# Kernel tuning notes

Hardware: AMD Instinct MI355X
Metric: run time of the kernel (lower is better)

Reference implementation:

```python
import jax, jax.numpy as jnp
import numpy as np

B, N, C_IN = 4, 120000, 4
FEAT, H, W = 128, 128, 128
PC_RANGE = (-50.0, -50.0, -5.0, 50.0, 50.0, 3.0)
EPS = 1e-5  # BatchNorm eps (torch default)


def setup_inputs() -> dict:
    key = jax.random.key(0)
    ks = jax.random.split(key, 16)
    # LiDAR-like point cloud: x,y spread ~[-90,90] (mostly in-range), z ~[-6,6], intensity ~N(0,1)
    points = jax.random.normal(ks[0], (B, N, C_IN), jnp.float32) * jnp.array([30.0, 30.0, 2.0, 1.0], jnp.float32)

    def lin(k, o, i):
        return jax.random.normal(k, (o, i), jnp.float32) * (1.0 / np.sqrt(i))

    def bn(k, c):
        k1, k2, k3, k4 = jax.random.split(k, 4)
        return (jax.random.normal(k1, (c,), jnp.float32) * 0.1 + 1.0,  # gamma
                jax.random.normal(k2, (c,), jnp.float32) * 0.1,        # beta
                jax.random.normal(k3, (c,), jnp.float32) * 0.1,        # running mean
                jax.random.uniform(k4, (c,), jnp.float32, 0.5, 1.5))   # running var

    g1, be1, m1, v1 = bn(ks[3], 64)
    g2, be2, m2, v2 = bn(ks[4], 128)
    g3, be3, m3, v3 = bn(ks[5], FEAT)
    return {
        'points': points,
        'W1': lin(ks[6], 64, C_IN), 'b1': jax.random.normal(ks[7], (64,), jnp.float32) * 0.01,
        'g1': g1, 'be1': be1, 'm1': m1, 'v1': v1,
        'W2': lin(ks[8], 128, 64), 'b2': jax.random.normal(ks[9], (128,), jnp.float32) * 0.01,
        'g2': g2, 'be2': be2, 'm2': m2, 'v2': v2,
        'W3': lin(ks[10], FEAT, 128), 'b3': jax.random.normal(ks[11], (FEAT,), jnp.float32) * 0.01,
        'g3': g3, 'be3': be3, 'm3': m3, 'v3': v3,
    }


def _bn_relu(x, g, b, m, v):
    # eval-mode BatchNorm1d + ReLU, applied over last (channel) axis
    return jax.nn.relu((x - m) * jax.lax.rsqrt(v + EPS) * g + b)


def _forward(points, W1, b1, g1, be1, m1, v1, W2, b2, g2, be2, m2, v2, W3, b3, g3, be3, m3, v3):
    # Per-point MLP (1x1 convs == per-point linears): [B,N,4] -> [B,N,FEAT]
    h = _bn_relu(jnp.einsum('bni,oi->bno', points, W1) + b1, g1, be1, m1, v1)
    h = _bn_relu(jnp.einsum('bni,oi->bno', h, W2) + b2, g2, be2, m2, v2)
    feats = _bn_relu(jnp.einsum('bni,oi->bno', h, W3) + b3, g3, be3, m3, v3)  # [B,N,FEAT]

    x, y = points[..., 0], points[..., 1]
    x_norm = (x - PC_RANGE[0]) / (PC_RANGE[3] - PC_RANGE[0])
    y_norm = (y - PC_RANGE[1]) / (PC_RANGE[4] - PC_RANGE[1])
    valid = (x_norm >= 0) & (x_norm <= 1) & (y_norm >= 0) & (y_norm <= 1)  # [B,N]

    gx = jnp.clip((x_norm * (W - 1)).astype(jnp.int32), 0, W - 1)
    gy = jnp.clip((y_norm * (H - 1)).astype(jnp.int32), 0, H - 1)
    bidx = jnp.arange(B, dtype=jnp.int32)[:, None]
    # invalid points routed to a dummy segment B*H*W
    seg = jnp.where(valid, bidx * (H * W) + gy * W + gx, B * H * W)  # [B,N]

    bev = jax.ops.segment_max(feats.reshape(B * N, FEAT), seg.reshape(B * N),
                              num_segments=B * H * W + 1)  # [B*H*W+1, FEAT]
    bev = bev[:B * H * W]
    bev = jnp.where(jnp.isneginf(bev), jnp.zeros((), bev.dtype), bev)  # empty cells stay 0
    return bev.reshape(B, H, W, FEAT).transpose(0, 3, 1, 2)  # [B, FEAT, H, W]


def reference(points, W1, b1, g1, be1, m1, v1, W2, b2, g2, be2, m2, v2, W3, b3, g3, be3, m3, v3):
    return _forward(points, W1, b1, g1, be1, m1, v1, W2, b2, g2, be2, m2, v2, W3, b3, g3, be3, m3, v3)
```

## Files before the change

kernel.cpp:

```cpp
#include <hip/hip_runtime.h>
#include <hip/hip_fp16.h>

#define BB 4
#define NN 120000
#define FEAT 128
#define HH 128
#define WW 128
#define NPTS (BB*NN)
#define HW (HH*WW)

#define OW1    0
#define OB1    256
#define OW2P   320
#define OB2    4416
#define OW3P   4544
#define OB3    12736
#define OW3F   12864
#define OW2F   21056
#define OCNT   25152
#define OOFF   90688
#define ONV    156224
#define OCELLS 156288
#define OSIDX  636288
#define OSCELL 1116288
#define OFEATS 1596288
#define OBEV   1596288
#define BEV_ELEMS (BB*HW*FEAT)

#if defined(__has_builtin)
#if __has_builtin(__builtin_amdgcn_fdot2)
#define HAS_FDOT2 1
#endif
#endif

typedef _Float16 hv2 __attribute__((ext_vector_type(2)));
typedef _Float16 f16x8 __attribute__((ext_vector_type(8)));
typedef float    f32x4 __attribute__((ext_vector_type(4)));
typedef float    fv16  __attribute__((ext_vector_type(16)));

__device__ __forceinline__ unsigned pk2(float a, float b) {
    __half2 h = __floats2half2_rn(a, b);
    return __builtin_bit_cast(unsigned, h);
}

__device__ __forceinline__ float dot2(unsigned a, unsigned b, float c) {
#ifdef HAS_FDOT2
    return __builtin_amdgcn_fdot2(__builtin_bit_cast(hv2, a),
                                  __builtin_bit_cast(hv2, b), c, false);
#else
    __half2 ah = __builtin_bit_cast(__half2, a), bh = __builtin_bit_cast(__half2, b);
    c = fmaf(__low2float(ah), __low2float(bh), c);
    return fmaf(__high2float(ah), __high2float(bh), c);
#endif
}

__device__ __forceinline__ unsigned hmax2u(unsigned a, unsigned b) {
    unsigned al = a & 0xFFFFu, bl = b & 0xFFFFu;
    unsigned ah = a & 0xFFFF0000u, bh = b & 0xFFFF0000u;
    unsigned lo = (al > bl) ? al : bl;
    unsigned hi = (ah > bh) ? ah : bh;
    return lo | hi;
}

__global__ void fold_weights_k(
    const float* __restrict__ W1, const float* __restrict__ b1,
    const float* __restrict__ g1, const float* __restrict__ be1,
    const float* __restrict__ m1, const float* __restrict__ v1,
    const float* __restrict__ W2, const float* __restrict__ b2,
    const float* __restrict__ g2, const float* __restrict__ be2,
    const float* __restrict__ m2, const float* __restrict__ v2,
    const float* __restrict__ W3, const float* __restrict__ b3,
    const float* __restrict__ g3, const float* __restrict__ be3,
    const float* __restrict__ m3, const float* __restrict__ v3,
    float* __restrict__ wf)
{
    unsigned* wu = (unsigned*)wf;
    int idx = blockIdx.x * 256 + threadIdx.x;
    const float EPSV = 1e-5f;
    if (idx < 256) {
        int o = idx >> 2;
        float s = g1[o] * rsqrtf(v1[o] + EPSV);
        wf[OW1 + idx] = W1[idx] * s;
    } else if (idx < 320) {
        int o = idx - 256;
        float s = g1[o] * rsqrtf(v1[o] + EPSV);
        wf[idx] = (b1[o] - m1[o]) * s + be1[o];
    } else if (idx < 4416) {
        int j = idx - OW2P;
        int r = j >> 7, o = j & 127;
        float s = g2[o] * rsqrtf(v2[o] + EPSV);
        wu[idx] = pk2(W2[o * 64 + 2 * r] * s, W2[o * 64 + 2 * r + 1] * s);
    } else if (idx < 4544) {
        int o = idx - OB2;
        float s = g2[o] * rsqrtf(v2[o] + EPSV);
        wf[idx] = (b2[o] - m2[o]) * s + be2[o];
    } else if (idx < 12736) {
        int j = idx - OW3P;
        int ch = j >> 9, rem = j & 511;
        int r = rem >> 3, jj = rem & 7;
        int o = ch * 8 + jj;
        float s = g3[o] * rsqrtf(v3[o] + EPSV);
        wu[idx] = pk2(W3[o * 128 + 2 * r] * s, W3[o * 128 + 2 * r + 1] * s);
    } else if (idx < 12864) {
        int o = idx - OB3;
        float s = g3[o] * rsqrtf(v3[o] + EPSV);
        wf[idx] = (b3[o] - m3[o]) * s + be3[o];
    } else if (idx < 21056) {
        int u = idx - OW3F;
        int tile = u >> 8, w = u & 255;
        int l = w >> 2, q = w & 3;
        int n = (tile >> 2) * 16 + (l & 15);
        int k = (tile & 3) * 32 + ((l >> 4) << 3) + 2 * q;
        float s = g3[n] * rsqrtf(v3[n] + EPSV);
        wu[idx] = pk2(W3[n * 128 + k] * s, W3[n * 128 + k + 1] * s);
    } else if (idx < 25152) {
        int u = idx - OW2F;
        int tile = u >> 8, w = u & 255;
        int l = w >> 2, q = w & 3;
        int n = (tile >> 1) * 16 + (l & 15);
        int k = (tile & 1) * 32 + ((l >> 4) << 3) + 2 * q;
        float s = g2[n] * rsqrtf(v2[n] + EPSV);
        wu[idx] = pk2(W2[n * 64 + k] * s, W2[n * 64 + k + 1] * s);
    }
}

__global__ __launch_bounds__(256)
void cells_hist_k(const float4* __restrict__ pts, int* __restrict__ cells,
                  int* __restrict__ cnt)
{
    int tid = blockIdx.x * 256 + threadIdx.x;
    float4 p = pts[tid];
    float xn = (p.x - (-50.0f)) / (50.0f - (-50.0f));
    float yn = (p.y - (-50.0f)) / (50.0f - (-50.0f));
    bool valid = (xn >= 0.0f) && (xn <= 1.0f) && (yn >= 0.0f) && (yn <= 1.0f);
    int gx = min(max((int)(xn * 127.0f), 0), 127);
    int gy = min(max((int)(yn * 127.0f), 0), 127);
    int b = tid / NN;
    int cell = valid ? (b * HW + gy * WW + gx) : -1;
    cells[tid] = cell;
    if (valid) atomicAdd(&cnt[cell], 1);
}

__global__ __launch_bounds__(1024)
void scan_k(const int* __restrict__ cnt, int* __restrict__ off, int* __restrict__ nvp)
{
    __shared__ int wsum[16];
    int t = threadIdx.x;
    int lane = t & 63, w = t >> 6;
    int base = t * 64;
    int s = 0;
#pragma unroll 8
    for (int j = 0; j < 64; ++j) s += cnt[base + j];
    int v = s;
#pragma unroll
    for (int d = 1; d < 64; d <<= 1) {
        int u = __shfl_up(v, d);
        if (lane >= d) v += u;
    }
    if (lane == 63) wsum[w] = v;
    __syncthreads();
    if (t == 0) {
        int r = 0;
#pragma unroll
        for (int k = 0; k < 16; ++k) { int x = wsum[k]; wsum[k] = r; r += x; }
        nvp[0] = r;
    }
    __syncthreads();
    int excl = (v - s) + wsum[w];
    int r = excl;
#pragma unroll 8
    for (int j = 0; j < 64; ++j) { off[base + j] = r; r += cnt[base + j]; }
}

__global__ __launch_bounds__(256)
void scatter_idx_k(const int* __restrict__ cells, int* __restrict__ off,
                   int* __restrict__ sidx, int* __restrict__ scell)
{
    int tid = blockIdx.x * 256 + threadIdx.x;
    int c = cells[tid];
    if (c >= 0) {
        int pos = atomicAdd(&off[c], 1);
        sidx[pos] = tid;
        scell[pos] = c;
    }
}

__global__ __launch_bounds__(256)
void fused_mlp_k(const float4* __restrict__ pts, const float* __restrict__ wf,
                 const int* __restrict__ sidx, const int* __restrict__ nvp,
                 uint4* __restrict__ feats4)
{
    __shared__ __align__(16) _Float16 h1t[4][16 * 72];
    __shared__ __align__(16) _Float16 h2t[4][16 * 136];
    __shared__ __align__(16) _Float16 stg[4][16 * 136];
    const unsigned* wu = (const unsigned*)wf;
    const uint4* bf2 = (const uint4*)(wu + OW2F);
    const uint4* bf3 = (const uint4*)(wu + OW3F);
    const int tid = threadIdx.x, wv = tid >> 6, l = tid & 63;
    const int nv = nvp[0];
    const int M0 = (blockIdx.x * 4 + wv) * 16;
    if (M0 >= nv) return;
    const int l15 = l & 15, q = l >> 4;

    const int slot = M0 + l15;
    const int pidx = (slot < nv) ? sidx[slot] : 0;
    float4 p = pts[pidx];

    unsigned r0[8];
#pragma unroll
    for (int t = 0; t < 8; ++t) {
        int o = q * 16 + 2 * t;
        const float* wa = wf + OW1 + o * 4;
        float a = wf[OB1 + o], b = wf[OB1 + o + 1];
        a = fmaf(wa[0], p.x, a); a = fmaf(wa[1], p.y, a);
        a = fmaf(wa[2], p.z, a); a = fmaf(wa[3], p.w, a);
        b = fmaf(wa[4], p.x, b); b = fmaf(wa[5], p.y, b);
        b = fmaf(wa[6], p.z, b); b = fmaf(wa[7], p.w, b);
        r0[t] = pk2(fmaxf(a, 0.f), fmaxf(b, 0.f));
    }
    {
        uint4* dst = (uint4*)&h1t[wv][l15 * 72 + q * 16];
        uint4 v0; v0.x = r0[0]; v0.y = r0[1]; v0.z = r0[2]; v0.w = r0[3];
        uint4 v1; v1.x = r0[4]; v1.y = r0[5]; v1.z = r0[6]; v1.w = r0[7];
        dst[0] = v0; dst[1] = v1;
    }

    uint4 a2[2];
#pragma unroll
    for (int kt = 0; kt < 2; ++kt)
        a2[kt] = *(const uint4*)&h1t[wv][l15 * 72 + kt * 32 + q * 8];

#pragma unroll 1
    for (int nt = 0; nt < 8; ++nt) {
        f32x4 acc = {0.f, 0.f, 0.f, 0.f};
        acc = __builtin_amdgcn_mfma_f32_16x16x32_f16(
            __builtin_bit_cast(f16x8, a2[0]),
            __builtin_bit_cast(f16x8, bf2[(nt * 2 + 0) * 64 + l]), acc, 0, 0, 0);
        acc = __builtin_amdgcn_mfma_f32_16x16x32_f16(
            __builtin_bit_cast(f16x8, a2[1]),
            __builtin_bit_cast(f16x8, bf2[(nt * 2 + 1) * 64 + l]), acc, 0, 0, 0);
        float bias = wf[OB2 + nt * 16 + l15];
#pragma unroll
        for (int rr = 0; rr < 4; ++rr)
            h2t[wv][(q * 4 + rr) * 136 + nt * 16 + l15] =
                (_Float16)fmaxf(acc[rr] + bias, 0.f);
    }

    uint4 a3[4];
#pragma unroll
    for (int kt = 0; kt < 4; ++kt)
        a3[kt] = *(const uint4*)&h2t[wv][l15 * 136 + kt * 32 + q * 8];

#pragma unroll 1
    for (int nt = 0; nt < 8; ++nt) {
        f32x4 acc = {0.f, 0.f, 0.f, 0.f};
#pragma unroll
        for (int kt = 0; kt < 4; ++kt)
            acc = __builtin_amdgcn_mfma_f32_16x16x32_f16(
                __builtin_bit_cast(f16x8, a3[kt]),
                __builtin_bit_cast(f16x8, bf3[(nt * 4 + kt) * 64 + l]), acc, 0, 0, 0);
        float bias = wf[OB3 + nt * 16 + l15];
#pragma unroll
        for (int rr = 0; rr < 4; ++rr)
            stg[wv][(q * 4 + rr) * 136 + nt * 16 + l15] =
                (_Float16)fmaxf(acc[rr] + bias, 0.f);
    }

    const int pt = l >> 2, part = l & 3;
#pragma unroll
    for (int i = 0; i < 4; ++i) {
        uint4 vv = *(const uint4*)&stg[wv][pt * 136 + (part * 4 + i) * 8];
        feats4[(size_t)(M0 + pt) * 16 + part * 4 + i] = vv;
    }
}

__global__ __launch_bounds__(256)
void reduce_k(const unsigned* __restrict__ feats, const int* __restrict__ off,
              const int* __restrict__ cnt, float* __restrict__ out)
{
    __shared__ float tile[128][65];
    const int tid = threadIdx.x;
    const int w = tid >> 6, l = tid & 63;
    const int l15 = l & 15, lq = l >> 4;
    const int c0 = blockIdx.x * 64;
    const uint4* f4 = (const uint4*)feats;

#pragma unroll 1
    for (int cc = 0; cc < 16; ++cc) {
        int c = c0 + w * 16 + cc;
        int n = cnt[c];
        int start = off[c] - n;
        uint4 m = {0u, 0u, 0u, 0u};
        const uint4* fp = f4 + (size_t)(start + lq) * 16 + l15;
#pragma unroll 1
        for (int p = 0; p < n; p += 4) {
            if (p + lq < n) {
                uint4 v = fp[(size_t)p * 16];
                m.x = hmax2u(m.x, v.x); m.y = hmax2u(m.y, v.y);
                m.z = hmax2u(m.z, v.z); m.w = hmax2u(m.w, v.w);
            }
        }
#pragma unroll
        for (int d = 16; d <= 32; d <<= 1) {
            m.x = hmax2u(m.x, (unsigned)__shfl_xor((int)m.x, d));
            m.y = hmax2u(m.y, (unsigned)__shfl_xor((int)m.y, d));
            m.z = hmax2u(m.z, (unsigned)__shfl_xor((int)m.z, d));
            m.w = hmax2u(m.w, (unsigned)__shfl_xor((int)m.w, d));
        }
        if (lq == 0) {
            int f0 = 8 * l15, cl = w * 16 + cc;
            __half2 hx = __builtin_bit_cast(__half2, m.x);
            __half2 hy = __builtin_bit_cast(__half2, m.y);
            __half2 hz = __builtin_bit_cast(__half2, m.z);
            __half2 hw = __builtin_bit_cast(__half2, m.w);
            tile[f0 + 0][cl] = __low2float(hx); tile[f0 + 1][cl] = __high2float(hx);
            tile[f0 + 2][cl] = __low2float(hy); tile[f0 + 3][cl] = __high2float(hy);
            tile[f0 + 4][cl] = __low2float(hz); tile[f0 + 5][cl] = __high2float(hz);
            tile[f0 + 6][cl] = __low2float(hw); tile[f0 + 7][cl] = __high2float(hw);
        }
    }
    __syncthreads();
    const int b = c0 >> 14;
    const int cxy = c0 & (HW - 1);
#pragma unroll 4
    for (int k = 0; k < 32; ++k) {
        int idx = k * 256 + tid;
        int f = idx >> 6, cl = idx & 63;
        out[((size_t)(b * 128 + f)) * HW + cxy + cl] = tile[f][cl];
    }
}

#define DPPMAX(A, D, S) { \
    float _pv = __int_as_float(__builtin_amdgcn_update_dpp( \
        0, __float_as_int(A), 0x110 | (D), 0xF, 0xF, false)); \
    A = (S) ? fmaxf(A, _pv) : A; }

__global__ __launch_bounds__(256)
void mlp_atomic_k(const float4* __restrict__ pts, const float* __restrict__ wf,
                  const int* __restrict__ sidx, const int* __restrict__ scell,
                  const int* __restrict__ nvp, float* __restrict__ bev, int layout)
{
    __shared__ unsigned h1s[32 * 256];
    __shared__ unsigned h2s[64 * 256];
    const unsigned* wu = (const unsigned*)wf;
    const int tid = threadIdx.x;
    const int slot = blockIdx.x * 256 + tid;
    const int nv = nvp[0];
    if ((slot & ~63) >= nv) return;
    const int lane = tid & 63;
    const int l15 = lane & 15;
    const bool live = slot < nv;
    const int cell = live ? scell[slot] : -1;
    const int pidx = live ? sidx[slot] : 0;
    float4 p = pts[pidx];

    int c1 = __shfl_up(cell, 1), c2 = __shfl_up(cell, 2);
    int c4 = __shfl_up(cell, 4), c8 = __shfl_up(cell, 8);
    bool s1 = (l15 >= 1) && (c1 == cell);
    bool s2 = (l15 >= 2) && (c2 == cell);
    bool s4 = (l15 >= 4) && (c4 == cell);
    bool s8 = (l15 >= 8) && (c8 == cell);
    int cn = __shfl_down(cell, 1);
    bool tail = (l15 == 15) || (cn != cell);

#pragma unroll
    for (int i = 0; i < 32; ++i) {
        const float* wa = wf + OW1 + 8 * i;
        float a = wf[OB1 + 2 * i], b = wf[OB1 + 2 * i + 1];
        a = fmaf(wa[0], p.x, a); a = fmaf(wa[1], p.y, a);
        a = fmaf(wa[2], p.z, a); a = fmaf(wa[3], p.w, a);
        b = fmaf(wa[4], p.x, b); b = fmaf(wa[5], p.y, b);
        b = fmaf(wa[6], p.z, b); b = fmaf(wa[7], p.w, b);
        h1s[i * 256 + tid] = pk2(fmaxf(a, 0.0f), fmaxf(b, 0.0f));
    }
#pragma unroll 1
    for (int o0 = 0; o0 < 128; o0 += 16) {
        fv16 acc;
#pragma unroll
        for (int j = 0; j < 16; ++j) acc[j] = wf[OB2 + o0 + j];
#pragma unroll
        for (int r = 0; r < 32; ++r) {
            unsigned h1r = h1s[r * 256 + tid];
            const unsigned* wr = wu + OW2P + r * 128 + o0;
#pragma unroll
            for (int j = 0; j < 16; ++j) acc[j] = dot2(h1r, wr[j], acc[j]);
        }
#pragma unroll
        for (int j = 0; j < 16; j += 2)
            h2s[((o0 + j) >> 1) * 256 + tid] =
                pk2(fmaxf(acc[j], 0.f), fmaxf(acc[j + 1], 0.f));
    }

    int* ob = (int*)bev;
    long base0;
    if (layout == 0) base0 = (long)cell * 128;
    else             base0 = (long)(cell >> 14) * (128 * HW) + (cell & (HW - 1));

#pragma unroll 1
    for (int ch = 0; ch < 16; ++ch) {
        float a0=wf[OB3+ch*8+0], a1=wf[OB3+ch*8+1], a2=wf[OB3+ch*8+2], a3=wf[OB3+ch*8+3];
        float a4=wf[OB3+ch*8+4], a5=wf[OB3+ch*8+5], a6=wf[OB3+ch*8+6], a7=wf[OB3+ch*8+7];
        const unsigned* wq = wu + OW3P + ch * 512;
#pragma unroll
        for (int r = 0; r < 64; ++r) {
            unsigned h2r = h2s[r * 256 + tid];
            a0 = dot2(h2r, wq[r*8+0], a0); a1 = dot2(h2r, wq[r*8+1], a1);
            a2 = dot2(h2r, wq[r*8+2], a2); a3 = dot2(h2r, wq[r*8+3], a3);
            a4 = dot2(h2r, wq[r*8+4], a4); a5 = dot2(h2r, wq[r*8+5], a5);
            a6 = dot2(h2r, wq[r*8+6], a6); a7 = dot2(h2r, wq[r*8+7], a7);
        }
        float av[8] = {a0,a1,a2,a3,a4,a5,a6,a7};
#pragma unroll
        for (int j = 0; j < 8; ++j) {
            float aj = fmaxf(av[j], 0.0f);
            DPPMAX(aj, 1, s1); DPPMAX(aj, 2, s2);
            DPPMAX(aj, 4, s4); DPPMAX(aj, 8, s8);
            av[j] = aj;
        }
        if (tail && cell >= 0) {
            if (layout == 0) {
#pragma unroll
                for (int j = 0; j < 8; ++j)
                    atomicMax(ob + base0 + ch * 8 + j, __float_as_int(av[j]));
            } else {
#pragma unroll
                for (int j = 0; j < 8; ++j)
                    atomicMax(ob + base0 + (long)(ch * 8 + j) * HW, __float_as_int(av[j]));
            }
        }
    }
}

__global__ void transpose_bev_k(const float* __restrict__ bev, float* __restrict__ out)
{
    __shared__ float tile[32][129];
    const int tid = threadIdx.x;
    const int cell0 = blockIdx.x * 32;
#pragma unroll
    for (int k = 0; k < 16; ++k) {
        int idx = k * 256 + tid;
        int c = idx >> 7, f = idx & 127;
        tile[c][f] = bev[(size_t)(cell0 + c) * 128 + f];
    }
    __syncthreads();
    const int b = cell0 >> 14;
    const int cl0 = cell0 & (HW - 1);
#pragma unroll
    for (int k = 0; k < 16; ++k) {
        int idx = k * 256 + tid;
        int f = idx >> 5, c = idx & 31;
        out[(size_t)(b * 128 + f) * HW + cl0 + c] = tile[c][f];
    }
}

extern "C" void kernel_launch(void* const* d_in, const int* in_sizes, int n_in,
                              void* d_out, int out_size, void* d_ws, size_t ws_size,
                              hipStream_t stream)
{
    const float* points = (const float*)d_in[0];
    const float* W1 = (const float*)d_in[1];  const float* b1 = (const float*)d_in[2];
    const float* g1 = (const float*)d_in[3];  const float* be1 = (const float*)d_in[4];
    const float* m1 = (const float*)d_in[5];  const float* v1 = (const float*)d_in[6];
    const float* W2 = (const float*)d_in[7];  const float* b2 = (const float*)d_in[8];
    const float* g2 = (const float*)d_in[9];  const float* be2 = (const float*)d_in[10];
    const float* m2 = (const float*)d_in[11]; const float* v2 = (const float*)d_in[12];
    const float* W3 = (const float*)d_in[13]; const float* b3 = (const float*)d_in[14];
    const float* g3 = (const float*)d_in[15]; const float* be3 = (const float*)d_in[16];
    const float* m3 = (const float*)d_in[17]; const float* v3 = (const float*)d_in[18];

    float* wsf = (float*)d_ws;
    int*   wsi = (int*)d_ws;
    const size_t need_full = ((size_t)OFEATS + (size_t)NPTS * 64) * 4;
    const size_t need_bev  = ((size_t)OBEV + BEV_ELEMS) * 4;

    fold_weights_k<<<99, 256, 0, stream>>>(
        W1, b1, g1, be1, m1, v1, W2, b2, g2, be2, m2, v2, W3, b3, g3, be3, m3, v3, wsf);

    (void)hipMemsetAsync(wsi + OCNT, 0, 65536 * sizeof(int), stream);
    cells_hist_k<<<NPTS / 256, 256, 0, stream>>>(
        (const float4*)points, wsi + OCELLS, wsi + OCNT);
    scan_k<<<1, 1024, 0, stream>>>(wsi + OCNT, wsi + OOFF, wsi + ONV);
    scatter_idx_k<<<NPTS / 256, 256, 0, stream>>>(
        wsi + OCELLS, wsi + OOFF, wsi + OSIDX, wsi + OSCELL);

    if (ws_size >= need_full) {
        uint4* feats4 = (uint4*)(wsi + OFEATS);
        fused_mlp_k<<<NPTS / 64, 256, 0, stream>>>(
            (const float4*)points, wsf, wsi + OSIDX, wsi + ONV, feats4);
        reduce_k<<<BB * HW / 64, 256, 0, stream>>>(
            (const unsigned*)feats4, wsi + OOFF, wsi + OCNT, (float*)d_out);
    } else if (ws_size >= need_bev) {
        float* bev = wsf + OBEV;
        (void)hipMemsetAsync(bev, 0, (size_t)BEV_ELEMS * sizeof(float), stream);
        mlp_atomic_k<<<NPTS / 256, 256, 0, stream>>>(
            (const float4*)points, wsf, wsi + OSIDX, wsi + OSCELL, wsi + ONV, bev, 0);
        transpose_bev_k<<<HW * BB / 32, 256, 0, stream>>>(bev, (float*)d_out);
    } else {
        (void)hipMemsetAsync(d_out, 0, (size_t)out_size * sizeof(float), stream);
        mlp_atomic_k<<<NPTS / 256, 256, 0, stream>>>(
            (const float4*)points, wsf, wsi + OSIDX, wsi + OSCELL, wsi + ONV,
            (float*)d_out, 1);
    }
}
```

Measured before the change: 289.3 us.

## Fold count memset into weight-fold kernel and slim MLP shared-memory staging

Zeroes the cell-count histogram inside fold_weights_k, removing a separate memset launch. In fused_mlp_k, the layer-1 outputs are built directly in MFMA A-operand registers, so the h1 shared-memory round trip goes away. Adjacent lanes pair their fp16 results through a DPP swap so each lane writes packed 32-bit words, and one padded buffer is reused for both h2 and the output staging. Unroll factors are also raised in the MLP and reduce loops, which may add register pressure.

Result: faster. 277.4 us (-4.1%).

```diff
diff --git a/kernel.cpp b/kernel.cpp
--- a/kernel.cpp
+++ b/kernel.cpp
@@ -60,6 +60,11 @@
     unsigned lo = (al > bl) ? al : bl;
     unsigned hi = (ah > bh) ? ah : bh;
     return lo | hi;
+}
+
+__device__ __forceinline__ unsigned h16(float v) {
+    _Float16 h = (_Float16)v;
+    return (unsigned)__builtin_bit_cast(unsigned short, h);
 }
 
 __global__ void fold_weights_k(
@@ -121,6 +126,8 @@
         int k = (tile & 1) * 32 + ((l >> 4) << 3) + 2 * q;
         float s = g2[n] * rsqrtf(v2[n] + EPSV);
         wu[idx] = pk2(W2[n * 64 + k] * s, W2[n * 64 + k + 1] * s);
+    } else if (idx < 25152 + 65536) {
+        ((int*)wf)[OCNT + idx - 25152] = 0;
     }
 }
 
@@ -190,9 +197,7 @@
                  const int* __restrict__ sidx, const int* __restrict__ nvp,
                  uint4* __restrict__ feats4)
 {
-    __shared__ __align__(16) _Float16 h1t[4][16 * 72];
-    __shared__ __align__(16) _Float16 h2t[4][16 * 136];
-    __shared__ __align__(16) _Float16 stg[4][16 * 136];
+    __shared__ __align__(16) _Float16 h2t[4][16 * 132];
     const unsigned* wu = (const unsigned*)wf;
     const uint4* bf2 = (const uint4*)(wu + OW2F);
     const uint4* bf3 = (const uint4*)(wu + OW3F);
@@ -201,36 +206,34 @@
     const int M0 = (blockIdx.x * 4 + wv) * 16;
     if (M0 >= nv) return;
     const int l15 = l & 15, q = l >> 4;
+    const int par = l15 & 1;
 
     const int slot = M0 + l15;
     const int pidx = (slot < nv) ? sidx[slot] : 0;
     float4 p = pts[pidx];
 
-    unsigned r0[8];
-#pragma unroll
-    for (int t = 0; t < 8; ++t) {
-        int o = q * 16 + 2 * t;
-        const float* wa = wf + OW1 + o * 4;
-        float a = wf[OB1 + o], b = wf[OB1 + o + 1];
-        a = fmaf(wa[0], p.x, a); a = fmaf(wa[1], p.y, a);
-        a = fmaf(wa[2], p.z, a); a = fmaf(wa[3], p.w, a);
-        b = fmaf(wa[4], p.x, b); b = fmaf(wa[5], p.y, b);
-        b = fmaf(wa[6], p.z, b); b = fmaf(wa[7], p.w, b);
-        r0[t] = pk2(fmaxf(a, 0.f), fmaxf(b, 0.f));
-    }
-    {
-        uint4* dst = (uint4*)&h1t[wv][l15 * 72 + q * 16];
-        uint4 v0; v0.x = r0[0]; v0.y = r0[1]; v0.z = r0[2]; v0.w = r0[3];
-        uint4 v1; v1.x = r0[4]; v1.y = r0[5]; v1.z = r0[6]; v1.w = r0[7];
-        dst[0] = v0; dst[1] = v1;
-    }
-
     uint4 a2[2];
 #pragma unroll
-    for (int kt = 0; kt < 2; ++kt)
-        a2[kt] = *(const uint4*)&h1t[wv][l15 * 72 + kt * 32 + q * 8];
-
-#pragma unroll 1
+    for (int kt = 0; kt < 2; ++kt) {
+        unsigned w4[4];
+#pragma unroll
+        for (int t = 0; t < 4; ++t) {
+            int f = kt * 32 + q * 8 + 2 * t;
+            const float* wa = wf + OW1 + f * 4;
+            float a = wf[OB1 + f], b = wf[OB1 + f + 1];
+            a = fmaf(wa[0], p.x, a); a = fmaf(wa[1], p.y, a);
+            a = fmaf(wa[2], p.z, a); a = fmaf(wa[3], p.w, a);
+            b = fmaf(wa[4], p.x, b); b = fmaf(wa[5], p.y, b);
+            b = fmaf(wa[6], p.z, b); b = fmaf(wa[7], p.w, b);
+            w4[t] = pk2(fmaxf(a, 0.f), fmaxf(b, 0.f));
+        }
+        uint4 v; v.x = w4[0]; v.y = w4[1]; v.z = w4[2]; v.w = w4[3];
+        a2[kt] = v;
+    }
+
+    unsigned* myh2 = (unsigned*)&h2t[wv][0];
+
+#pragma unroll
     for (int nt = 0; nt < 8; ++nt) {
         f32x4 acc = {0.f, 0.f, 0.f, 0.f};
         acc = __builtin_amdgcn_mfma_f32_16x16x32_f16(
@@ -240,18 +243,28 @@
             __builtin_bit_cast(f16x8, a2[1]),
             __builtin_bit_cast(f16x8, bf2[(nt * 2 + 1) * 64 + l]), acc, 0, 0, 0);
         float bias = wf[OB2 + nt * 16 + l15];
-#pragma unroll
-        for (int rr = 0; rr < 4; ++rr)
-            h2t[wv][(q * 4 + rr) * 136 + nt * 16 + l15] =
-                (_Float16)fmaxf(acc[rr] + bias, 0.f);
+        unsigned wrd[4];
+#pragma unroll
+        for (int rr = 0; rr < 4; ++rr) {
+            unsigned h = h16(fmaxf(acc[rr] + bias, 0.f));
+            unsigned nb = (unsigned)__builtin_amdgcn_update_dpp(
+                0, (int)h, 0xB1 , 0xF, 0xF, false);
+            wrd[rr] = par ? ((nb & 0xFFFFu) | (h << 16)) : (h | (nb << 16));
+        }
+        unsigned* base = myh2 + nt * 8 + (l15 >> 1);
+#pragma unroll
+        for (int i = 0; i < 2; ++i) {
+            int rr = 2 * par + i;
+            base[(q * 4 + rr) * 66] = wrd[rr];
+        }
     }
 
     uint4 a3[4];
 #pragma unroll
     for (int kt = 0; kt < 4; ++kt)
-        a3[kt] = *(const uint4*)&h2t[wv][l15 * 136 + kt * 32 + q * 8];
-
-#pragma unroll 1
+        a3[kt] = *(const uint4*)&h2t[wv][l15 * 132 + kt * 32 + q * 8];
+
+#pragma unroll 2
     for (int nt = 0; nt < 8; ++nt) {
         f32x4 acc = {0.f, 0.f, 0.f, 0.f};
 #pragma unroll
@@ -260,16 +273,26 @@
                 __builtin_bit_cast(f16x8, a3[kt]),
                 __builtin_bit_cast(f16x8, bf3[(nt * 4 + kt) * 64 + l]), acc, 0, 0, 0);
         float bias = wf[OB3 + nt * 16 + l15];
-#pragma unroll
-        for (int rr = 0; rr < 4; ++rr)
-            stg[wv][(q * 4 + rr) * 136 + nt * 16 + l15] =
-                (_Float16)fmaxf(acc[rr] + bias, 0.f);
+        unsigned wrd[4];
+#pragma unroll
+        for (int rr = 0; rr < 4; ++rr) {
+            unsigned h = h16(fmaxf(acc[rr] + bias, 0.f));
+            unsigned nb = (unsigned)__builtin_amdgcn_update_dpp(
+                0, (int)h, 0xB1, 0xF, 0xF, false);
+            wrd[rr] = par ? ((nb & 0xFFFFu) | (h << 16)) : (h | (nb << 16));
+        }
+        unsigned* base = myh2 + nt * 8 + (l15 >> 1);
+#pragma unroll
+        for (int i = 0; i < 2; ++i) {
+            int rr = 2 * par + i;
+            base[(q * 4 + rr) * 66] = wrd[rr];
+        }
     }
 
     const int pt = l >> 2, part = l & 3;
 #pragma unroll
     for (int i = 0; i < 4; ++i) {
-        uint4 vv = *(const uint4*)&stg[wv][pt * 136 + (part * 4 + i) * 8];
+        uint4 vv = *(const uint4*)&h2t[wv][pt * 132 + (part * 4 + i) * 8];
         feats4[(size_t)(M0 + pt) * 16 + part * 4 + i] = vv;
     }
 }
@@ -285,7 +308,7 @@
     const int c0 = blockIdx.x * 64;
     const uint4* f4 = (const uint4*)feats;
 
-#pragma unroll 1
+#pragma unroll 2
     for (int cc = 0; cc < 16; ++cc) {
         int c = c0 + w * 16 + cc;
         int n = cnt[c];
@@ -473,10 +496,9 @@
     const size_t need_full = ((size_t)OFEATS + (size_t)NPTS * 64) * 4;
     const size_t need_bev  = ((size_t)OBEV + BEV_ELEMS) * 4;
 
-    fold_weights_k<<<99, 256, 0, stream>>>(
+    fold_weights_k<<<(25152 + 65536 + 255) / 256, 256, 0, stream>>>(
         W1, b1, g1, be1, m1, v1, W2, b2, g2, be2, m2, v2, W3, b3, g3, be3, m3, v3, wsf);
 
-    (void)hipMemsetAsync(wsi + OCNT, 0, 65536 * sizeof(int), stream);
     cells_hist_k<<<NPTS / 256, 256, 0, stream>>>(
         (const float4*)points, wsi + OCELLS, wsi + OCNT);
     scan_k<<<1, 1024, 0, stream>>>(wsi + OCNT, wsi + OOFF, wsi + ONV);
```
